# Kernel tuning notes

Hardware: AMD Instinct MI355X
Metric: run time of the kernel (lower is better)

Reference implementation:

```python
import jax, jax.numpy as jnp
import numpy as np

N_SRC, N_DST, E, F = 100000, 50000, 1250000, 64


def setup_inputs() -> dict:
    key = jax.random.key(0)
    ks = jax.random.split(key, 11)
    return {
        "hidden_feat": jax.random.normal(ks[0], (N_SRC, F), jnp.float32),
        "node_feat_src": jax.random.normal(ks[1], (N_SRC, F), jnp.float32),
        "node_feat_dst": jax.random.normal(ks[2], (N_DST, F), jnp.float32),
        "norm_deg_src": jax.random.uniform(ks[3], (N_SRC,), jnp.float32),
        "norm_deg_dst": jax.random.uniform(ks[4], (N_DST,), jnp.float32),
        # q_probs are importance-sampling probabilities; keep bounded away from 0
        "q_probs": jax.random.uniform(ks[5], (N_SRC,), jnp.float32) + 0.5,
        "sample_weights": jax.random.normal(ks[6], (F, 2), jnp.float32),
        "fc_weight": jax.random.normal(ks[7], (F, F), jnp.float32) * 0.1,
        "fc_bias": jax.random.normal(ks[8], (F,), jnp.float32) * 0.1,
        "src_idx": jax.random.randint(ks[9], (E,), 0, N_SRC, jnp.int32),
        "dst_idx": jax.random.randint(ks[10], (E,), 0, N_DST, jnp.int32),
    }


def reference(hidden_feat, node_feat_src, node_feat_dst, norm_deg_src,
              norm_deg_dst, q_probs, sample_weights, fc_weight, fc_bias,
              src_idx, dst_idx):
    n_dst = norm_deg_dst.shape[0]
    n_edges = src_idx.shape[0]
    # per-node projections, then edge gather (same math as per-edge matmul)
    hu = node_feat_src @ sample_weights[:, 0]  # [N_src]
    hv = node_feat_dst @ sample_weights[:, 1]  # [N_dst]
    att = (norm_deg_src[src_idx] * norm_deg_dst[dst_idx]
           * (jax.nn.relu(hu[src_idx] + hv[dst_idx]) + 0.1)
           / q_probs[src_idx] / n_edges)                     # [E]
    msg = hidden_feat[src_idx] * att[:, None]                # [E, F]
    neigh = jax.ops.segment_sum(msg, dst_idx, num_segments=n_dst)  # [N_dst, F]
    rst = neigh @ fc_weight.T + fc_bias
    return rst
```

## Files before the change

### kernel.cpp

```cpp
#include <hip/hip_runtime.h>
#include <hip/hip_bf16.h>
#include <hip/hip_fp16.h>

#define N_SRC 100000
#define N_DST 50000
#define N_EDGE 1250000
#define F 64

#define BINWC 128
#define NBINC 391
#define BCAPC 4096
#define BINWF 32
#define NBINF 1563
#define DCAP 80
#define EPB 4096

#define PART_BLOCKS 306
#define PROJ_BLOCKS 9375
#define CVT_BLOCKS  3125
#define CVTW_BLOCKS 16

#define ATT_SCALE     65536.0f
#define INV_ATT_SCALE (1.0f/65536.0f)

#define NSTRIDE 65

__device__ __forceinline__ unsigned int fp4nib(float x) {
    float ax = fabsf(x);
    unsigned m = (unsigned)(ax > 0.25f) + (ax > 0.75f) + (ax > 1.25f) + (ax > 1.75f)
               + (ax > 2.5f) + (ax > 3.5f) + (ax > 5.0f);
    return ((x < 0.0f) ? 8u : 0u) | m;
}
#define TABLO 0x3E3C3800u
#define TABHI 0x46444240u

__device__ __forceinline__ unsigned short f2bf(float x) {
    unsigned b = __float_as_uint(x);
    return (unsigned short)((b + 0x7FFF + ((b >> 16) & 1)) >> 16);
}
__device__ __forceinline__ float bf2f(unsigned short u) {
    return __uint_as_float(((unsigned)u) << 16);
}
__device__ __forceinline__ int h2i(__half2 h) { union { __half2 h; int i; } u; u.h = h; return u.i; }
__device__ __forceinline__ __half2 i2h(int i) { union { __half2 h; int i; } u; u.i = i; return u.h; }
__device__ __forceinline__ unsigned h16bits(float x) {
    union { __half h; unsigned short u; } v; v.h = __float2half(x); return v.u;
}

__device__ __forceinline__ void fp4_fma(unsigned r0, __half2 av,
        __half2& a01, __half2& a23, __half2& a45, __half2& a67) {
    unsigned selL = r0 & 0x07070707u;
    unsigned selH = (r0 >> 4) & 0x07070707u;
    unsigned hbl  = __builtin_amdgcn_perm(TABHI, TABLO, selL)
                  | ((r0 << 4) & 0x80808080u);
    unsigned hbh  = __builtin_amdgcn_perm(TABHI, TABLO, selH)
                  | (r0 & 0x80808080u);
    a01 = __hfma2(i2h((int)(((hbl & 0x000000FFu) << 8)
                          | ((hbh & 0x000000FFu) << 24))), av, a01);
    a23 = __hfma2(i2h((int)(( hbl & 0x0000FF00u)
                          | ((hbh & 0x0000FF00u) << 16))), av, a23);
    a45 = __hfma2(i2h((int)(((hbl >> 8) & 0x0000FF00u)
                          | ((hbh << 8) & 0xFF000000u))), av, a45);
    a67 = __hfma2(i2h((int)(((hbl >> 16) & 0x0000FF00u)
                          | ( hbh & 0xFF000000u))), av, a67);
}

__global__ __launch_bounds__(256) void prep_part_kernel(
        const float* __restrict__ nfs,
        const float* __restrict__ nfd,
        const float* __restrict__ sw,
        const float* __restrict__ nds,
        const float* __restrict__ q,
        const float* __restrict__ hidden,
        const float* __restrict__ W,
        const int* __restrict__ src_idx,
        const int* __restrict__ dst_idx,
        float2* __restrict__ husrc,
        float* __restrict__ hv,
        int* __restrict__ cursor,
        int* __restrict__ coarse,
        unsigned int* __restrict__ hfp4,
        unsigned short* __restrict__ Wbf) {
    __shared__ int hist[NBINC];
    __shared__ int gbase[NBINC];
    __shared__ float w0[F], w1[F];
    int tid = threadIdx.x;
    int b = blockIdx.x;
    if (b < PART_BLOCKS) {
        for (int i = tid; i < NBINC; i += 256) hist[i] = 0;
        __syncthreads();
        int e0 = b * EPB;
        int pack[16], meta[16];
        #pragma unroll
        for (int i = 0; i < 16; ++i) {
            int e = e0 + i * 256 + tid;
            meta[i] = -1; pack[i] = 0;
            if (e < N_EDGE) {
                int s = src_idx[e], d = dst_idx[e];
                int bin = d >> 7, ld = d & 127;
                int r = atomicAdd(&hist[bin], 1);
                pack[i] = (ld << 24) | s;
                meta[i] = (bin << 12) | r;
            }
        }
        __syncthreads();
        for (int i = tid; i < NBINC; i += 256) {
            int h = hist[i];
            gbase[i] = h ? atomicAdd(&cursor[i], h) : 0;
        }
        __syncthreads();
        #pragma unroll
        for (int i = 0; i < 16; ++i) {
            if (meta[i] >= 0) {
                int bin = meta[i] >> 12, r = meta[i] & 0xFFF;
                int pos = gbase[bin] + r;
                if (pos < BCAPC) coarse[bin * BCAPC + pos] = pack[i];
            }
        }
    } else if (b < PART_BLOCKS + PROJ_BLOCKS) {
        if (tid < 2 * F) {
            float v = sw[tid];
            if (tid & 1) w1[tid >> 1] = v; else w0[tid >> 1] = v;
        }
        __syncthreads();
        int r  = (b - PART_BLOCKS) * 16 + (tid >> 4);
        int c4 = tid & 15;
        float4 x; const float* w;
        if (r < N_SRC) { x = ((const float4*)(nfs + (size_t)r * F))[c4]; w = w0; }
        else           { x = ((const float4*)(nfd + (size_t)(r - N_SRC) * F))[c4]; w = w1; }
        float s = x.x * w[c4*4] + x.y * w[c4*4+1] + x.z * w[c4*4+2] + x.w * w[c4*4+3];
        s += __shfl_xor(s, 1, 64);
        s += __shfl_xor(s, 2, 64);
        s += __shfl_xor(s, 4, 64);
        s += __shfl_xor(s, 8, 64);
        if (c4 == 0) {
            if (r < N_SRC)
                husrc[r] = make_float2(s, nds[r] * (ATT_SCALE / (float)N_EDGE) / q[r]);
            else
                hv[r - N_SRC] = s;
        }
    } else if (b < PART_BLOCKS + PROJ_BLOCKS + CVT_BLOCKS) {
        int c = (b - PART_BLOCKS - PROJ_BLOCKS) * 256 + tid;
        const float4* h4 = (const float4*)hidden;
        float4 a = h4[2 * c], d = h4[2 * c + 1];
        unsigned int o =  fp4nib(a.x)        | (fp4nib(a.y) << 4)
                       | (fp4nib(a.z) << 8)  | (fp4nib(a.w) << 12)
                       | (fp4nib(d.x) << 16) | (fp4nib(d.y) << 20)
                       | (fp4nib(d.z) << 24) | (fp4nib(d.w) << 28);
        hfp4[c] = o;
    } else {
        int idx = (b - PART_BLOCKS - PROJ_BLOCKS - CVT_BLOCKS) * 256 + tid;
        Wbf[idx] = f2bf(W[idx]);
    }
}

typedef short bf16x8 __attribute__((ext_vector_type(8)));
typedef float f32x4  __attribute__((ext_vector_type(4)));

__global__ __launch_bounds__(256) void bin_gather_fc_kernel(
        const unsigned int* __restrict__ hfp4,
        const int* __restrict__ cursor,
        const int* __restrict__ coarse,
        const float2* __restrict__ husrc,
        const float* __restrict__ hv,
        const float* __restrict__ ndd,
        const unsigned short* __restrict__ Wbf,
        const float* __restrict__ bias,
        float* __restrict__ out) {
    __shared__ unsigned int slat[BINWF * DCAP];
    __shared__ int dcnt[BINWF];
    __shared__ float hvl[BINWF], nddl[BINWF];
    __shared__ float neigh[BINWF][NSTRIDE];
    int tid = threadIdx.x;
    int bin = blockIdx.x;
    int sub = bin & 3;
    int parent = bin >> 2;
    int d0  = bin * BINWF;
    if (tid < BINWF) {
        dcnt[tid] = 0;
        int d = d0 + tid;
        if (d < N_DST) { hvl[tid] = hv[d]; nddl[tid] = ndd[d]; }
    }
    __syncthreads();
    int cnt = cursor[parent]; if (cnt > BCAPC) cnt = BCAPC;
    int base = parent * BCAPC;
    for (int i = tid; i < cnt; i += 256) {
        unsigned p = (unsigned)coarse[base + i];
        unsigned ld7 = p >> 24;
        if ((int)(ld7 >> 5) != sub) continue;
        int s  = (int)(p & 0xFFFFFF);
        int ld = (int)(ld7 & 31);
        float2 hc = husrc[s];
        float att = hc.y * nddl[ld] * (fmaxf(hc.x + hvl[ld], 0.0f) + 0.1f);
        int pos = atomicAdd(&dcnt[ld], 1);
        if (pos < DCAP)
            slat[ld * DCAP + pos] = (h16bits(att) << 17) | (unsigned)s;
    }
    __syncthreads();
    int wv = tid >> 6, lane = tid & 63;
    int esub = lane & 7, dwi = lane >> 3;
    const __half2 hz = __floats2half2_rn(0.f, 0.f);
    for (int t = 0; t < 8; t += 2) {
        int ldA = wv * 8 + t;
        int ldB = ldA + 1;
        int nA = dcnt[ldA]; if (nA > DCAP) nA = DCAP;
        int nB = dcnt[ldB]; if (nB > DCAP) nB = DCAP;
        int bA = ldA * DCAP, bB = ldB * DCAP;
        __half2 A01 = hz, A23 = hz, A45 = hz, A67 = hz;
        __half2 B01 = hz, B23 = hz, B45 = hz, B67 = hz;
        int nmax = nA > nB ? nA : nB;
        for (int g = 0; g < nmax; g += 32) {
            unsigned rwA[4], rwB[4]; __half2 avA[4], avB[4];
            #pragma unroll
            for (int k = 0; k < 4; ++k) {
                int idx = g + k * 8 + esub;
                unsigned pA = (idx < nA) ? slat[bA + idx] : 0u;
                unsigned pB = (idx < nB) ? slat[bB + idx] : 0u;
                unsigned abA = pA >> 17;
                unsigned abB = pB >> 17;
                avA[k] = i2h((int)(abA | (abA << 16)));
                avB[k] = i2h((int)(abB | (abB << 16)));
                rwA[k] = hfp4[(size_t)(pA & 0x1FFFFu) * 8 + dwi];
                rwB[k] = hfp4[(size_t)(pB & 0x1FFFFu) * 8 + dwi];
            }
            #pragma unroll
            for (int k = 0; k < 4; ++k) {
                fp4_fma(rwA[k], avA[k], A01, A23, A45, A67);
                fp4_fma(rwB[k], avB[k], B01, B23, B45, B67);
            }
        }
        #pragma unroll
        for (int off = 1; off < 8; off <<= 1) {
            A01 = __hadd2(A01, i2h(__shfl_xor(h2i(A01), off, 64)));
            A23 = __hadd2(A23, i2h(__shfl_xor(h2i(A23), off, 64)));
            A45 = __hadd2(A45, i2h(__shfl_xor(h2i(A45), off, 64)));
            A67 = __hadd2(A67, i2h(__shfl_xor(h2i(A67), off, 64)));
            B01 = __hadd2(B01, i2h(__shfl_xor(h2i(B01), off, 64)));
            B23 = __hadd2(B23, i2h(__shfl_xor(h2i(B23), off, 64)));
            B45 = __hadd2(B45, i2h(__shfl_xor(h2i(B45), off, 64)));
            B67 = __hadd2(B67, i2h(__shfl_xor(h2i(B67), off, 64)));
        }
        __half2 selA = (esub < 4) ? ((esub < 2) ? A01 : A23)
                                  : ((esub < 6) ? A45 : A67);
        __half2 selB = (esub < 4) ? ((esub < 2) ? B01 : B23)
                                  : ((esub < 6) ? B45 : B67);
        float vA = (esub & 1) ? __high2float(selA) : __low2float(selA);
        float vB = (esub & 1) ? __high2float(selB) : __low2float(selB);
        neigh[ldA][lane] = vA * INV_ATT_SCALE;
        neigh[ldB][lane] = vB * INV_ATT_SCALE;
    }
    __syncthreads();
    int row = lane & 15, quad = lane >> 4;
    int m0 = (wv >> 1) * 16;
    int nt0 = (wv & 1) * 2;
#if __has_builtin(__builtin_amdgcn_mfma_f32_16x16x32_bf16)
    const float* arow = &neigh[m0 + row][0];
    bf16x8 a0, a1;
    #pragma unroll
    for (int j = 0; j < 8; ++j) {
        a0[j] = (short)f2bf(arow[quad * 8 + j]);
        a1[j] = (short)f2bf(arow[32 + quad * 8 + j]);
    }
    #pragma unroll
    for (int k = 0; k < 2; ++k) {
        int nt = nt0 + k;
        bf16x8 b0 = *(const bf16x8*)(Wbf + (size_t)(nt * 16 + row) * F + quad * 8);
        bf16x8 b1 = *(const bf16x8*)(Wbf + (size_t)(nt * 16 + row) * F + 32 + quad * 8);
        f32x4 c = {0.f, 0.f, 0.f, 0.f};
        c = __builtin_amdgcn_mfma_f32_16x16x32_bf16(a0, b0, c, 0, 0, 0);
        c = __builtin_amdgcn_mfma_f32_16x16x32_bf16(a1, b1, c, 0, 0, 0);
        float bi = bias[nt * 16 + row];
        #pragma unroll
        for (int r = 0; r < 4; ++r) {
            int m = d0 + m0 + quad * 4 + r;
            if (m < N_DST) out[(size_t)m * F + nt * 16 + row] = c[r] + bi;
        }
    }
#else
    int r = tid >> 3, cg = tid & 7;
    int m = d0 + r;
    if (m < N_DST) {
        #pragma unroll
        for (int cc = 0; cc < 8; ++cc) {
            int c = cg * 8 + cc;
            float acc = bias[c];
            for (int k = 0; k < F; ++k)
                acc += neigh[r][k] * bf2f(Wbf[(size_t)c * F + k]);
            out[(size_t)m * F + c] = acc;
        }
    }
    (void)row; (void)quad; (void)m0; (void)nt0;
#endif
}

static inline char* align16(char* p) {
    return (char*)(((uintptr_t)p + 15) & ~(uintptr_t)15);
}

extern "C" void kernel_launch(void* const* d_in, const int* in_sizes, int n_in,
                              void* d_out, int out_size, void* d_ws, size_t ws_size,
                              hipStream_t stream) {
    const float* hidden_feat   = (const float*)d_in[0];
    const float* node_feat_src = (const float*)d_in[1];
    const float* node_feat_dst = (const float*)d_in[2];
    const float* norm_deg_src  = (const float*)d_in[3];
    const float* norm_deg_dst  = (const float*)d_in[4];
    const float* q_probs       = (const float*)d_in[5];
    const float* sample_w      = (const float*)d_in[6];
    const float* fc_weight     = (const float*)d_in[7];
    const float* fc_bias       = (const float*)d_in[8];
    const int*   src_idx       = (const int*)d_in[9];
    const int*   dst_idx       = (const int*)d_in[10];
    float* out = (float*)d_out;

    char* ws = (char*)d_ws;
    int*    coarse = (int*)ws;    ws = align16(ws + sizeof(int) * (size_t)NBINC * BCAPC);
    float2* husrc  = (float2*)ws; ws = align16(ws + sizeof(float2) * N_SRC);
    float*  hv     = (float*)ws;  ws = align16(ws + sizeof(float) * N_DST);
    int*    cursor = (int*)ws;    ws = align16(ws + sizeof(int) * NBINC);
    unsigned int*   hfp4 = (unsigned int*)ws;
                                  ws = align16(ws + sizeof(int) * (size_t)N_SRC * F / 8);
    unsigned short* Wbf  = (unsigned short*)ws;
                                  ws = align16(ws + sizeof(short) * F * F);

    hipMemsetAsync(cursor, 0, sizeof(int) * NBINC, stream);

    prep_part_kernel<<<PART_BLOCKS + PROJ_BLOCKS + CVT_BLOCKS + CVTW_BLOCKS,
                       256, 0, stream>>>(
        node_feat_src, node_feat_dst, sample_w, norm_deg_src, q_probs,
        hidden_feat, fc_weight, src_idx, dst_idx,
        husrc, hv, cursor, coarse, hfp4, Wbf);
    bin_gather_fc_kernel<<<NBINF, 256, 0, stream>>>(hfp4, cursor, coarse,
                                                    husrc, hv, norm_deg_dst,
                                                    Wbf, fc_bias, out);
}
```

Baseline: 167.8 us.

## Replace two-level coarse binning with direct per-destination global slot lists

Removes the coarse 128-wide bin partitioning and the per-block LDS re-bucketing. A new edge kernel computes attention per edge and appends a packed (att, src) entry straight into a per-destination global slot array using global atomics on a per-destination cursor. The gather kernel then reads those slots directly from global memory. This drops the shared-memory second pass and the filtering of three quarters of the coarse entries per block, at the cost of an extra kernel launch, many contended global atomics, and scattered 4-byte global writes.

```diff
diff --git a/kernel.cpp b/kernel.cpp
--- a/kernel.cpp
+++ b/kernel.cpp
@@ -7,18 +7,14 @@
 #define N_EDGE 1250000
 #define F 64
 
-#define BINWC 128
-#define NBINC 391
-#define BCAPC 4096
+#define DCAP 80
 #define BINWF 32
 #define NBINF 1563
-#define DCAP 80
-#define EPB 4096
-
-#define PART_BLOCKS 306
+
 #define PROJ_BLOCKS 9375
 #define CVT_BLOCKS  3125
 #define CVTW_BLOCKS 16
+#define EDGE_BLOCKS 1221
 
 #define ATT_SCALE     65536.0f
 #define INV_ATT_SCALE (1.0f/65536.0f)
@@ -65,65 +61,29 @@
                           | ( hbh & 0xFF000000u))), av, a67);
 }
 
-__global__ __launch_bounds__(256) void prep_part_kernel(
+__global__ __launch_bounds__(256) void prep_kernel(
         const float* __restrict__ nfs,
         const float* __restrict__ nfd,
         const float* __restrict__ sw,
         const float* __restrict__ nds,
         const float* __restrict__ q,
+        const float* __restrict__ ndd,
         const float* __restrict__ hidden,
         const float* __restrict__ W,
-        const int* __restrict__ src_idx,
-        const int* __restrict__ dst_idx,
         float2* __restrict__ husrc,
-        float* __restrict__ hv,
-        int* __restrict__ cursor,
-        int* __restrict__ coarse,
+        float2* __restrict__ hvd,
         unsigned int* __restrict__ hfp4,
         unsigned short* __restrict__ Wbf) {
-    __shared__ int hist[NBINC];
-    __shared__ int gbase[NBINC];
     __shared__ float w0[F], w1[F];
     int tid = threadIdx.x;
     int b = blockIdx.x;
-    if (b < PART_BLOCKS) {
-        for (int i = tid; i < NBINC; i += 256) hist[i] = 0;
-        __syncthreads();
-        int e0 = b * EPB;
-        int pack[16], meta[16];
-        #pragma unroll
-        for (int i = 0; i < 16; ++i) {
-            int e = e0 + i * 256 + tid;
-            meta[i] = -1; pack[i] = 0;
-            if (e < N_EDGE) {
-                int s = src_idx[e], d = dst_idx[e];
-                int bin = d >> 7, ld = d & 127;
-                int r = atomicAdd(&hist[bin], 1);
-                pack[i] = (ld << 24) | s;
-                meta[i] = (bin << 12) | r;
-            }
-        }
-        __syncthreads();
-        for (int i = tid; i < NBINC; i += 256) {
-            int h = hist[i];
-            gbase[i] = h ? atomicAdd(&cursor[i], h) : 0;
-        }
-        __syncthreads();
-        #pragma unroll
-        for (int i = 0; i < 16; ++i) {
-            if (meta[i] >= 0) {
-                int bin = meta[i] >> 12, r = meta[i] & 0xFFF;
-                int pos = gbase[bin] + r;
-                if (pos < BCAPC) coarse[bin * BCAPC + pos] = pack[i];
-            }
-        }
-    } else if (b < PART_BLOCKS + PROJ_BLOCKS) {
+    if (b < PROJ_BLOCKS) {
         if (tid < 2 * F) {
             float v = sw[tid];
             if (tid & 1) w1[tid >> 1] = v; else w0[tid >> 1] = v;
         }
         __syncthreads();
-        int r  = (b - PART_BLOCKS) * 16 + (tid >> 4);
+        int r  = b * 16 + (tid >> 4);
         int c4 = tid & 15;
         float4 x; const float* w;
         if (r < N_SRC) { x = ((const float4*)(nfs + (size_t)r * F))[c4]; w = w0; }
@@ -134,13 +94,15 @@
         s += __shfl_xor(s, 4, 64);
         s += __shfl_xor(s, 8, 64);
         if (c4 == 0) {
-            if (r < N_SRC)
+            if (r < N_SRC) {
                 husrc[r] = make_float2(s, nds[r] * (ATT_SCALE / (float)N_EDGE) / q[r]);
-            else
-                hv[r - N_SRC] = s;
-        }
-    } else if (b < PART_BLOCKS + PROJ_BLOCKS + CVT_BLOCKS) {
-        int c = (b - PART_BLOCKS - PROJ_BLOCKS) * 256 + tid;
+            } else {
+                int d = r - N_SRC;
+                hvd[d] = make_float2(s, ndd[d]);
+            }
+        }
+    } else if (b < PROJ_BLOCKS + CVT_BLOCKS) {
+        int c = (b - PROJ_BLOCKS) * 256 + tid;
         const float4* h4 = (const float4*)hidden;
         float4 a = h4[2 * c], d = h4[2 * c + 1];
         unsigned int o =  fp4nib(a.x)        | (fp4nib(a.y) << 4)
@@ -149,63 +111,59 @@
                        | (fp4nib(d.z) << 24) | (fp4nib(d.w) << 28);
         hfp4[c] = o;
     } else {
-        int idx = (b - PART_BLOCKS - PROJ_BLOCKS - CVT_BLOCKS) * 256 + tid;
+        int idx = (b - PROJ_BLOCKS - CVT_BLOCKS) * 256 + tid;
         Wbf[idx] = f2bf(W[idx]);
+    }
+}
+
+__global__ __launch_bounds__(256) void edge_att_kernel(
+        const int* __restrict__ src_idx,
+        const int* __restrict__ dst_idx,
+        const float2* __restrict__ husrc,
+        const float2* __restrict__ hvd,
+        int* __restrict__ cursor,
+        unsigned int* __restrict__ slat) {
+    int tid = threadIdx.x;
+    int e0 = blockIdx.x * 1024;
+    #pragma unroll
+    for (int i = 0; i < 4; ++i) {
+        int e = e0 + i * 256 + tid;
+        if (e < N_EDGE) {
+            int s = src_idx[e], d = dst_idx[e];
+            float2 hc = husrc[s];
+            float2 hd = hvd[d];
+            float att = hc.y * hd.y * (fmaxf(hc.x + hd.x, 0.0f) + 0.1f);
+            int pos = atomicAdd(&cursor[d], 1);
+            if (pos < DCAP)
+                slat[(size_t)d * DCAP + pos] = (h16bits(att) << 17) | (unsigned)s;
+        }
     }
 }
 
 typedef short bf16x8 __attribute__((ext_vector_type(8)));
 typedef float f32x4  __attribute__((ext_vector_type(4)));
 
-__global__ __launch_bounds__(256) void bin_gather_fc_kernel(
+__global__ __launch_bounds__(256) void gather_fc_kernel(
         const unsigned int* __restrict__ hfp4,
         const int* __restrict__ cursor,
-        const int* __restrict__ coarse,
-        const float2* __restrict__ husrc,
-        const float* __restrict__ hv,
-        const float* __restrict__ ndd,
+        const unsigned int* __restrict__ slat,
         const unsigned short* __restrict__ Wbf,
         const float* __restrict__ bias,
         float* __restrict__ out) {
-    __shared__ unsigned int slat[BINWF * DCAP];
-    __shared__ int dcnt[BINWF];
-    __shared__ float hvl[BINWF], nddl[BINWF];
     __shared__ float neigh[BINWF][NSTRIDE];
     int tid = threadIdx.x;
     int bin = blockIdx.x;
-    int sub = bin & 3;
-    int parent = bin >> 2;
     int d0  = bin * BINWF;
-    if (tid < BINWF) {
-        dcnt[tid] = 0;
-        int d = d0 + tid;
-        if (d < N_DST) { hvl[tid] = hv[d]; nddl[tid] = ndd[d]; }
-    }
-    __syncthreads();
-    int cnt = cursor[parent]; if (cnt > BCAPC) cnt = BCAPC;
-    int base = parent * BCAPC;
-    for (int i = tid; i < cnt; i += 256) {
-        unsigned p = (unsigned)coarse[base + i];
-        unsigned ld7 = p >> 24;
-        if ((int)(ld7 >> 5) != sub) continue;
-        int s  = (int)(p & 0xFFFFFF);
-        int ld = (int)(ld7 & 31);
-        float2 hc = husrc[s];
-        float att = hc.y * nddl[ld] * (fmaxf(hc.x + hvl[ld], 0.0f) + 0.1f);
-        int pos = atomicAdd(&dcnt[ld], 1);
-        if (pos < DCAP)
-            slat[ld * DCAP + pos] = (h16bits(att) << 17) | (unsigned)s;
-    }
-    __syncthreads();
     int wv = tid >> 6, lane = tid & 63;
     int esub = lane & 7, dwi = lane >> 3;
     const __half2 hz = __floats2half2_rn(0.f, 0.f);
     for (int t = 0; t < 8; t += 2) {
         int ldA = wv * 8 + t;
         int ldB = ldA + 1;
-        int nA = dcnt[ldA]; if (nA > DCAP) nA = DCAP;
-        int nB = dcnt[ldB]; if (nB > DCAP) nB = DCAP;
-        int bA = ldA * DCAP, bB = ldB * DCAP;
+        int dA = d0 + ldA, dB = d0 + ldB;
+        int nA = (dA < N_DST) ? cursor[dA] : 0; if (nA > DCAP) nA = DCAP;
+        int nB = (dB < N_DST) ? cursor[dB] : 0; if (nB > DCAP) nB = DCAP;
+        size_t bA = (size_t)dA * DCAP, bB = (size_t)dB * DCAP;
         __half2 A01 = hz, A23 = hz, A45 = hz, A67 = hz;
         __half2 B01 = hz, B23 = hz, B45 = hz, B67 = hz;
         int nmax = nA > nB ? nA : nB;
@@ -314,23 +272,23 @@
     float* out = (float*)d_out;
 
     char* ws = (char*)d_ws;
-    int*    coarse = (int*)ws;    ws = align16(ws + sizeof(int) * (size_t)NBINC * BCAPC);
+    unsigned int* slat = (unsigned int*)ws;
+                                  ws = align16(ws + sizeof(int) * (size_t)N_DST * DCAP);
     float2* husrc  = (float2*)ws; ws = align16(ws + sizeof(float2) * N_SRC);
-    float*  hv     = (float*)ws;  ws = align16(ws + sizeof(float) * N_DST);
-    int*    cursor = (int*)ws;    ws = align16(ws + sizeof(int) * NBINC);
+    float2* hvd    = (float2*)ws; ws = align16(ws + sizeof(float2) * N_DST);
+    int*    cursor = (int*)ws;    ws = align16(ws + sizeof(int) * N_DST);
     unsigned int*   hfp4 = (unsigned int*)ws;
                                   ws = align16(ws + sizeof(int) * (size_t)N_SRC * F / 8);
     unsigned short* Wbf  = (unsigned short*)ws;
                                   ws = align16(ws + sizeof(short) * F * F);
 
-    hipMemsetAsync(cursor, 0, sizeof(int) * NBINC, stream);
-
-    prep_part_kernel<<<PART_BLOCKS + PROJ_BLOCKS + CVT_BLOCKS + CVTW_BLOCKS,
-                       256, 0, stream>>>(
+    hipMemsetAsync(cursor, 0, sizeof(int) * N_DST, stream);
+
+    prep_kernel<<<PROJ_BLOCKS + CVT_BLOCKS + CVTW_BLOCKS, 256, 0, stream>>>(
         node_feat_src, node_feat_dst, sample_w, norm_deg_src, q_probs,
-        hidden_feat, fc_weight, src_idx, dst_idx,
-        husrc, hv, cursor, coarse, hfp4, Wbf);
-    bin_gather_fc_kernel<<<NBINF, 256, 0, stream>>>(hfp4, cursor, coarse,
-                                                    husrc, hv, norm_deg_dst,
-                                                    Wbf, fc_bias, out);
-}
+        norm_deg_dst, hidden_feat, fc_weight, husrc, hvd, hfp4, Wbf);
+    edge_att_kernel<<<EDGE_BLOCKS, 256, 0, stream>>>(
+        src_idx, dst_idx, husrc, hvd, cursor, slat);
+    gather_fc_kernel<<<NBINF, 256, 0, stream>>>(hfp4, cursor, slat,
+                                                Wbf, fc_bias, out);
+}
```

Measured after the change: 225.2 us. +34.2%, slower.

## Split fine binning into separate repartition kernel writing per-destination edge lists

Applied to the files above, without the earlier changes.

Moves the per-destination attention computation and fine bucketing out of the gather kernel into a new repartition kernel. That kernel reads each coarse bin once and writes packed per-destination slot arrays to global memory. Previously each of four sub-blocks scanned the whole parent bin and kept a quarter of it. The coarse bins are also widened to 256 destinations, and hv and norm_deg_dst are packed into one float2. This removes the 4x redundant scan of coarse bins but adds a kernel launch and a global write/read round trip for the slot lists. Larger coarse bins also reduce parallelism in the repartition step to 196 blocks.

```diff
diff --git a/kernel.cpp b/kernel.cpp
--- a/kernel.cpp
+++ b/kernel.cpp
@@ -7,12 +7,12 @@
 #define N_EDGE 1250000
 #define F 64
 
-#define BINWC 128
-#define NBINC 391
-#define BCAPC 4096
+#define BINWC 256
+#define NBINC 196
+#define BCAPC 8192
+#define DCAP 80
 #define BINWF 32
 #define NBINF 1563
-#define DCAP 80
 #define EPB 4096
 
 #define PART_BLOCKS 306
@@ -71,12 +71,13 @@
         const float* __restrict__ sw,
         const float* __restrict__ nds,
         const float* __restrict__ q,
+        const float* __restrict__ ndd,
         const float* __restrict__ hidden,
         const float* __restrict__ W,
         const int* __restrict__ src_idx,
         const int* __restrict__ dst_idx,
         float2* __restrict__ husrc,
-        float* __restrict__ hv,
+        float2* __restrict__ hvd,
         int* __restrict__ cursor,
         int* __restrict__ coarse,
         unsigned int* __restrict__ hfp4,
@@ -87,7 +88,7 @@
     int tid = threadIdx.x;
     int b = blockIdx.x;
     if (b < PART_BLOCKS) {
-        for (int i = tid; i < NBINC; i += 256) hist[i] = 0;
+        if (tid < NBINC) hist[tid] = 0;
         __syncthreads();
         int e0 = b * EPB;
         int pack[16], meta[16];
@@ -97,16 +98,16 @@
             meta[i] = -1; pack[i] = 0;
             if (e < N_EDGE) {
                 int s = src_idx[e], d = dst_idx[e];
-                int bin = d >> 7, ld = d & 127;
+                int bin = d >> 8, ld = d & 255;
                 int r = atomicAdd(&hist[bin], 1);
                 pack[i] = (ld << 24) | s;
                 meta[i] = (bin << 12) | r;
             }
         }
         __syncthreads();
-        for (int i = tid; i < NBINC; i += 256) {
-            int h = hist[i];
-            gbase[i] = h ? atomicAdd(&cursor[i], h) : 0;
+        if (tid < NBINC) {
+            int h = hist[tid];
+            gbase[tid] = h ? atomicAdd(&cursor[tid], h) : 0;
         }
         __syncthreads();
         #pragma unroll
@@ -134,10 +135,12 @@
         s += __shfl_xor(s, 4, 64);
         s += __shfl_xor(s, 8, 64);
         if (c4 == 0) {
-            if (r < N_SRC)
+            if (r < N_SRC) {
                 husrc[r] = make_float2(s, nds[r] * (ATT_SCALE / (float)N_EDGE) / q[r]);
-            else
-                hv[r - N_SRC] = s;
+            } else {
+                int d = r - N_SRC;
+                hvd[d] = make_float2(s, ndd[d]);
+            }
         }
     } else if (b < PART_BLOCKS + PROJ_BLOCKS + CVT_BLOCKS) {
         int c = (b - PART_BLOCKS - PROJ_BLOCKS) * 256 + tid;
@@ -154,58 +157,67 @@
     }
 }
 
-typedef short bf16x8 __attribute__((ext_vector_type(8)));
-typedef float f32x4  __attribute__((ext_vector_type(4)));
-
-__global__ __launch_bounds__(256) void bin_gather_fc_kernel(
-        const unsigned int* __restrict__ hfp4,
+__global__ __launch_bounds__(1024) void repart_kernel(
         const int* __restrict__ cursor,
         const int* __restrict__ coarse,
         const float2* __restrict__ husrc,
-        const float* __restrict__ hv,
-        const float* __restrict__ ndd,
+        const float2* __restrict__ hvd,
+        int* __restrict__ dcnt,
+        unsigned int* __restrict__ slat) {
+    __shared__ int lcnt[BINWC];
+    __shared__ float hvl[BINWC], nddl[BINWC];
+    int tid = threadIdx.x;
+    int parent = blockIdx.x;
+    int d0 = parent * BINWC;
+    if (tid < BINWC) {
+        lcnt[tid] = 0;
+        int d = d0 + tid;
+        if (d < N_DST) { float2 h = hvd[d]; hvl[tid] = h.x; nddl[tid] = h.y; }
+    }
+    __syncthreads();
+    int cnt = cursor[parent]; if (cnt > BCAPC) cnt = BCAPC;
+    size_t base = (size_t)parent * BCAPC;
+    for (int i = tid; i < cnt; i += 1024) {
+        unsigned p = (unsigned)coarse[base + i];
+        unsigned s = p & 0x1FFFFu;
+        int ld = (int)(p >> 24);
+        float2 hc = husrc[s];
+        float att = hc.y * nddl[ld] * (fmaxf(hc.x + hvl[ld], 0.0f) + 0.1f);
+        int pos = atomicAdd(&lcnt[ld], 1);
+        if (pos < DCAP)
+            slat[(size_t)(d0 + ld) * DCAP + pos] = (h16bits(att) << 17) | s;
+    }
+    __syncthreads();
+    if (tid < BINWC) {
+        int d = d0 + tid;
+        if (d < N_DST) { int n = lcnt[tid]; dcnt[d] = n > DCAP ? DCAP : n; }
+    }
+}
+
+typedef short bf16x8 __attribute__((ext_vector_type(8)));
+typedef float f32x4  __attribute__((ext_vector_type(4)));
+
+__global__ __launch_bounds__(256) void gather_fc_kernel(
+        const unsigned int* __restrict__ hfp4,
+        const int* __restrict__ dcnt,
+        const unsigned int* __restrict__ slat,
         const unsigned short* __restrict__ Wbf,
         const float* __restrict__ bias,
         float* __restrict__ out) {
-    __shared__ unsigned int slat[BINWF * DCAP];
-    __shared__ int dcnt[BINWF];
-    __shared__ float hvl[BINWF], nddl[BINWF];
     __shared__ float neigh[BINWF][NSTRIDE];
     int tid = threadIdx.x;
     int bin = blockIdx.x;
-    int sub = bin & 3;
-    int parent = bin >> 2;
     int d0  = bin * BINWF;
-    if (tid < BINWF) {
-        dcnt[tid] = 0;
-        int d = d0 + tid;
-        if (d < N_DST) { hvl[tid] = hv[d]; nddl[tid] = ndd[d]; }
-    }
-    __syncthreads();
-    int cnt = cursor[parent]; if (cnt > BCAPC) cnt = BCAPC;
-    int base = parent * BCAPC;
-    for (int i = tid; i < cnt; i += 256) {
-        unsigned p = (unsigned)coarse[base + i];
-        unsigned ld7 = p >> 24;
-        if ((int)(ld7 >> 5) != sub) continue;
-        int s  = (int)(p & 0xFFFFFF);
-        int ld = (int)(ld7 & 31);
-        float2 hc = husrc[s];
-        float att = hc.y * nddl[ld] * (fmaxf(hc.x + hvl[ld], 0.0f) + 0.1f);
-        int pos = atomicAdd(&dcnt[ld], 1);
-        if (pos < DCAP)
-            slat[ld * DCAP + pos] = (h16bits(att) << 17) | (unsigned)s;
-    }
-    __syncthreads();
     int wv = tid >> 6, lane = tid & 63;
     int esub = lane & 7, dwi = lane >> 3;
     const __half2 hz = __floats2half2_rn(0.f, 0.f);
     for (int t = 0; t < 8; t += 2) {
         int ldA = wv * 8 + t;
         int ldB = ldA + 1;
-        int nA = dcnt[ldA]; if (nA > DCAP) nA = DCAP;
-        int nB = dcnt[ldB]; if (nB > DCAP) nB = DCAP;
-        int bA = ldA * DCAP, bB = ldB * DCAP;
+        int dA = d0 + ldA, dB = d0 + ldB;
+        int nA = (dA < N_DST) ? dcnt[dA] : 0; if (nA > DCAP) nA = DCAP;
+        int nB = (dB < N_DST) ? dcnt[dB] : 0; if (nB > DCAP) nB = DCAP;
+        size_t bA = (size_t)dA * DCAP, bB = (size_t)dB * DCAP;
         __half2 A01 = hz, A23 = hz, A45 = hz, A67 = hz;
         __half2 B01 = hz, B23 = hz, B45 = hz, B67 = hz;
         int nmax = nA > nB ? nA : nB;
@@ -315,9 +327,12 @@
 
     char* ws = (char*)d_ws;
     int*    coarse = (int*)ws;    ws = align16(ws + sizeof(int) * (size_t)NBINC * BCAPC);
+    unsigned int* slat = (unsigned int*)ws;
+                                  ws = align16(ws + sizeof(int) * (size_t)N_DST * DCAP);
     float2* husrc  = (float2*)ws; ws = align16(ws + sizeof(float2) * N_SRC);
-    float*  hv     = (float*)ws;  ws = align16(ws + sizeof(float) * N_DST);
+    float2* hvd    = (float2*)ws; ws = align16(ws + sizeof(float2) * N_DST);
     int*    cursor = (int*)ws;    ws = align16(ws + sizeof(int) * NBINC);
+    int*    dcnt   = (int*)ws;    ws = align16(ws + sizeof(int) * N_DST);
     unsigned int*   hfp4 = (unsigned int*)ws;
                                   ws = align16(ws + sizeof(int) * (size_t)N_SRC * F / 8);
     unsigned short* Wbf  = (unsigned short*)ws;
@@ -328,9 +343,10 @@
     prep_part_kernel<<<PART_BLOCKS + PROJ_BLOCKS + CVT_BLOCKS + CVTW_BLOCKS,
                        256, 0, stream>>>(
         node_feat_src, node_feat_dst, sample_w, norm_deg_src, q_probs,
-        hidden_feat, fc_weight, src_idx, dst_idx,
-        husrc, hv, cursor, coarse, hfp4, Wbf);
-    bin_gather_fc_kernel<<<NBINF, 256, 0, stream>>>(hfp4, cursor, coarse,
-                                                    husrc, hv, norm_deg_dst,
-                                                    Wbf, fc_bias, out);
-}
+        norm_deg_dst, hidden_feat, fc_weight, src_idx, dst_idx,
+        husrc, hvd, cursor, coarse, hfp4, Wbf);
+    repart_kernel<<<NBINC, 1024, 0, stream>>>(cursor, coarse, husrc, hvd,
+                                              dcnt, slat);
+    gather_fc_kernel<<<NBINF, 256, 0, stream>>>(hfp4, dcnt, slat,
+                                                Wbf, fc_bias, out);
+}
```

Measured after the change: 180.8 us. 7.8% more time.
